# Performance work log

Measured on AMD Instinct MI355X. Metric: run time of the kernel, lower is better.

Reference implementation:

```python
import jax, jax.numpy as jnp
import numpy as np

HIDDEN = 1024
NUM_HEADS = 16
HEAD_DIM = 64
B, S = 2, 2048


def setup_inputs() -> dict:
    key = jax.random.key(0)
    k1, k2, k3 = jax.random.split(key, 3)
    x = jax.random.normal(k1, (B, S, HIDDEN), dtype=jnp.float32)
    # xavier-uniform style scaling for the projection weights
    lim_qkv = (6.0 / (HIDDEN + 3 * NUM_HEADS * HEAD_DIM)) ** 0.5
    lim_o = (6.0 / (NUM_HEADS * HEAD_DIM + HIDDEN)) ** 0.5
    w_qkv = jax.random.uniform(k2, (HIDDEN, 3 * NUM_HEADS * HEAD_DIM), jnp.float32, -lim_qkv, lim_qkv)
    w_o = jax.random.uniform(k3, (NUM_HEADS * HEAD_DIM, HIDDEN), jnp.float32, -lim_o, lim_o)
    return {"x": x, "w_qkv": w_qkv, "w_o": w_o}


def reference(x, w_qkv, w_o):
    b, s, _ = x.shape
    qkv = jnp.einsum('bsh,hf->bsf', x, w_qkv)               # [b, s, 3*H*D]
    qkv = qkv.reshape(b, s, 3, NUM_HEADS, HEAD_DIM)
    q = jnp.transpose(qkv[:, :, 0], (0, 2, 1, 3))           # [b, h, s, d]
    k = jnp.transpose(qkv[:, :, 1], (0, 2, 3, 1))           # [b, h, d, s]
    v = jnp.transpose(qkv[:, :, 2], (0, 2, 1, 3))           # [b, h, s, d]
    scores = jnp.einsum('bhqd,bhdk->bhqk', q, k) / jnp.sqrt(jnp.float32(HEAD_DIM))
    scores = jax.nn.softmax(scores, axis=-1)                # [b, h, q, k]
    # NOTE: faithful to source bug: sums over q, output indexed by k
    values = jnp.einsum('bhqk,bhkd->bhkd', scores, v)       # [b, h, s, d]
    values = jnp.transpose(values, (0, 2, 1, 3)).reshape(b, s, NUM_HEADS * HEAD_DIM)
    return jnp.einsum('bsf,fh->bsh', values, w_o)
```

## Files before the change

kernel.cpp:

```cpp
#include <hip/hip_runtime.h>
#include <stdint.h>


#define DEV static __device__ __forceinline__

typedef unsigned short u16;
typedef __attribute__((ext_vector_type(4))) float f32x4;
typedef __attribute__((ext_vector_type(16))) float f32x16;
typedef __bf16 bf16x8 __attribute__((ext_vector_type(8)));
typedef __attribute__((ext_vector_type(8))) unsigned short u16x8;
typedef __attribute__((ext_vector_type(4))) unsigned short u16x4;

#define QSCALE 0.18033688011112042f

DEV u16 f2bf(float f) {
    unsigned u = __builtin_bit_cast(unsigned, f);
    u += 0x7fffu + ((u >> 16) & 1u);
    return (u16)(u >> 16);
}
DEV float bf2f(u16 h) {
    unsigned u = ((unsigned)h) << 16;
    return __builtin_bit_cast(float, u);
}

DEV void async_copy16(const void* g, void* l) {
    __builtin_amdgcn_global_load_lds(
        (__attribute__((address_space(1))) void*)(g),
        (__attribute__((address_space(3))) void*)(l), 16, 0, 0);
}

DEV void transpose_tile(const float* __restrict__ src, u16* __restrict__ dst,
                        int rows, int cols, int bx, int by, int t, float* tile) {
    int c0 = bx * 32, r0 = by * 32;
    int tx = t & 31, ty = t >> 5;
#pragma unroll
    for (int i = 0; i < 4; i++)
        tile[(ty + i * 8) * 33 + tx] = src[(size_t)(r0 + ty + i * 8) * cols + c0 + tx];
    __syncthreads();
#pragma unroll
    for (int i = 0; i < 4; i++)
        dst[(size_t)(c0 + ty + i * 8) * rows + r0 + tx] = f2bf(tile[tx * 33 + ty + i * 8]);
}

__global__ __launch_bounds__(256) void prep(
    const float* __restrict__ x, const float* __restrict__ wqkv,
    const float* __restrict__ wo, u16* __restrict__ xb,
    u16* __restrict__ wqkvT, u16* __restrict__ woT) {
    __shared__ float tile[32 * 33];
    const int gid = blockIdx.x;
    const int t = threadIdx.x;
    if (gid < 4096) {
        int i = gid * 256 + t;
        f32x4 v = *(const f32x4*)(x + (size_t)i * 4);
        u16x4 o;
#pragma unroll
        for (int j = 0; j < 4; j++) o[j] = f2bf(v[j]);
        *(u16x4*)(xb + (size_t)i * 4) = o;
    } else if (gid < 7168) {
        int lid = gid - 4096;
        transpose_tile(wqkv, wqkvT, 1024, 3072, lid % 96, lid / 96, t, tile);
    } else {
        int lid = gid - 7168;
        transpose_tile(wo, woT, 1024, 1024, lid & 31, lid >> 5, t, tile);
    }
}

__global__ __launch_bounds__(256) void gemm_qkv(
    const u16* __restrict__ A, const u16* __restrict__ Bt,
    u16* __restrict__ qb, u16* __restrict__ kb, u16* __restrict__ vb) {
    __shared__ __align__(16) u16 smem[128 * 136];
    u16* As = smem;
    u16* Bs = smem + 4096;
    const int t = threadIdx.x;
    const int wave = t >> 6;
    const int lane = t & 63;
    const int quad = lane >> 4;
    const int l16 = lane & 15;
    const int wr = wave >> 1;
    const int wc = wave & 1;
    const int m0 = blockIdx.y * 128;
    const int n0 = blockIdx.x * 128;

    f32x4 acc[4][4];
#pragma unroll
    for (int i = 0; i < 4; i++)
#pragma unroll
        for (int j = 0; j < 4; j++) acc[i][j] = {0.f, 0.f, 0.f, 0.f};

    for (int kt = 0; kt < 1024; kt += 32) {
#pragma unroll
        for (int i = 0; i < 2; i++) {
            int idx = i * 256 + t;
            int row = idx >> 2, kc = idx & 3;
            async_copy16(A + (size_t)(m0 + row) * 1024 + kt + kc * 8, &As[idx * 8]);
            async_copy16(Bt + (size_t)(n0 + row) * 1024 + kt + kc * 8, &Bs[idx * 8]);
        }
        __syncthreads();
        bf16x8 af[4], bfr[4];
#pragma unroll
        for (int mt = 0; mt < 4; mt++)
            af[mt] = *(const bf16x8*)&As[(wr * 64 + mt * 16 + l16) * 32 + quad * 8];
#pragma unroll
        for (int nt = 0; nt < 4; nt++)
            bfr[nt] = *(const bf16x8*)&Bs[(wc * 64 + nt * 16 + l16) * 32 + quad * 8];
#pragma unroll
        for (int mt = 0; mt < 4; mt++)
#pragma unroll
            for (int nt = 0; nt < 4; nt++)
                acc[mt][nt] = __builtin_amdgcn_mfma_f32_16x16x32_bf16(
                    af[mt], bfr[nt], acc[mt][nt], 0, 0, 0);
        __syncthreads();
    }

    const int tsel = n0 >> 10;
    u16* dst = tsel == 0 ? qb : (tsel == 1 ? kb : vb);
    const float scl = tsel == 0 ? QSCALE : 1.0f;
#pragma unroll
    for (int mt = 0; mt < 4; mt++)
#pragma unroll
        for (int nt = 0; nt < 4; nt++) {
            int nn = wc * 64 + nt * 16 + l16;
#pragma unroll
            for (int r = 0; r < 4; r++) {
                int mm = wr * 64 + mt * 16 + quad * 4 + r;
                smem[mm * 136 + nn] = f2bf(acc[mt][nt][r] * scl);
            }
        }
    __syncthreads();
    const int col0 = (l16) * 8;
    const int rowb = (t >> 4);
    const int h0 = (n0 & 1023) >> 6;
#pragma unroll
    for (int i = 0; i < 8; i++) {
        int row = i * 16 + rowb;
        u16x8 v = *(const u16x8*)&smem[row * 136 + col0];
        int h = h0 + (col0 >> 6), d = col0 & 63;
        int mm = m0 + row;
        int b = mm >> 11, s = mm & 2047;
        *(u16x8*)&dst[((size_t)((b * 16 + h) * 2048 + s)) * 64 + d] = v;
    }
}

__global__ __launch_bounds__(256) void attn_pass1(
    const u16* __restrict__ qb, const u16* __restrict__ kb,
    float* __restrict__ lp) {
    __shared__ __align__(16) u16 Ks0[256 * 32];
    __shared__ __align__(16) u16 Ks1[256 * 32];
    const int t = threadIdx.x;
    const int wave = t >> 6;
    const int lane = t & 63;
    const int l32 = lane & 31, half = lane >> 5;
    const int kchunk = blockIdx.x & 1;
    const int qblk = (blockIdx.x >> 1) & 15;
    const int bh = blockIdx.x >> 5;
    const int q0 = qblk * 128 + wave * 32;

    const u16* Qr = qb + (size_t)(bh * 2048 + q0 + l32) * 64 + half * 8;
    bf16x8 a[4];
#pragma unroll
    for (int f = 0; f < 4; f++) a[f] = *(const bf16x8*)&Qr[f * 16];

    const u16* Kbase = kb + (size_t)(bh * 2048 + kchunk * 1024) * 64;
    const int srow = t >> 2, sc = (t & 3) * 8;

    float lsum[16];
#pragma unroll
    for (int r = 0; r < 16; r++) lsum[r] = 0.f;

    for (int kt = 0; kt < 4; kt++) {
#pragma unroll
        for (int rr = 0; rr < 4; rr++) {
            const u16* src = Kbase + (size_t)(kt * 256 + rr * 64 + srow) * 64 + sc;
            async_copy16(src, &Ks0[rr * 2048 + t * 8]);
            async_copy16(src + 32, &Ks1[rr * 2048 + t * 8]);
        }
        __syncthreads();
#pragma unroll
        for (int sub = 0; sub < 8; sub++) {
            const int row = sub * 32 + l32;
            bf16x8 bfr[4];
            bfr[0] = *(const bf16x8*)&Ks0[row * 32 + half * 8];
            bfr[1] = *(const bf16x8*)&Ks0[row * 32 + 16 + half * 8];
            bfr[2] = *(const bf16x8*)&Ks1[row * 32 + half * 8];
            bfr[3] = *(const bf16x8*)&Ks1[row * 32 + 16 + half * 8];
            f32x16 acc;
#pragma unroll
            for (int r = 0; r < 16; r++) acc[r] = 0.f;
#pragma unroll
            for (int f = 0; f < 4; f++)
                acc = __builtin_amdgcn_mfma_f32_32x32x16_bf16(a[f], bfr[f], acc, 0, 0, 0);
#pragma unroll
            for (int r = 0; r < 16; r++)
                lsum[r] += __builtin_amdgcn_exp2f(acc[r]);
        }
        __syncthreads();
    }
#pragma unroll
    for (int r = 0; r < 16; r++) {
        float v = lsum[r];
        v += __shfl_xor(v, 1);
        v += __shfl_xor(v, 2);
        v += __shfl_xor(v, 4);
        v += __shfl_xor(v, 8);
        v += __shfl_xor(v, 16);
        lsum[r] = v;
    }
    if (l32 == 0) {
        float* dst = lp + kchunk * 65536 + bh * 2048 + q0 + half * 4;
#pragma unroll
        for (int r = 0; r < 16; r++)
            dst[(r & 3) + 8 * (r >> 2)] = lsum[r];
    }
}

__global__ __launch_bounds__(256) void attn_pass2(
    const u16* __restrict__ qb, const u16* __restrict__ kb,
    const float* __restrict__ lp, float* __restrict__ cp) {
    __shared__ __align__(16) u16 Qs0[256 * 32];
    __shared__ __align__(16) u16 Qs1[256 * 32];
    __shared__ __align__(16) float li_lds[1024];
    const int t = threadIdx.x;
    const int wave = t >> 6;
    const int lane = t & 63;
    const int l32 = lane & 31, half = lane >> 5;
    const int qchunk = blockIdx.x & 1;
    const int kblk = (blockIdx.x >> 1) & 15;
    const int bh = blockIdx.x >> 5;
    const int k0 = kblk * 128 + wave * 32;

    {
        const int base = bh * 2048 + qchunk * 1024;
        f32x4 p0 = *(const f32x4*)&lp[base + t * 4];
        f32x4 p1 = *(const f32x4*)&lp[65536 + base + t * 4];
        f32x4 li;
#pragma unroll
        for (int j = 0; j < 4; j++) li[j] = 1.0f / (p0[j] + p1[j]);
        *(f32x4*)&li_lds[t * 4] = li;
    }

    const u16* Kr = kb + (size_t)(bh * 2048 + k0 + l32) * 64 + half * 8;
    bf16x8 b[4];
#pragma unroll
    for (int f = 0; f < 4; f++) b[f] = *(const bf16x8*)&Kr[f * 16];

    const u16* Qbase = qb + (size_t)(bh * 2048 + qchunk * 1024) * 64;
    const int srow = t >> 2, sc = (t & 3) * 8;

    float cs = 0.f;
    __syncthreads();

    for (int qt = 0; qt < 4; qt++) {
#pragma unroll
        for (int rr = 0; rr < 4; rr++) {
            const u16* src = Qbase + (size_t)(qt * 256 + rr * 64 + srow) * 64 + sc;
            async_copy16(src, &Qs0[rr * 2048 + t * 8]);
            async_copy16(src + 32, &Qs1[rr * 2048 + t * 8]);
        }
        __syncthreads();
#pragma unroll
        for (int sub = 0; sub < 8; sub++) {
            const int row = sub * 32 + l32;
            bf16x8 af[4];
            af[0] = *(const bf16x8*)&Qs0[row * 32 + half * 8];
            af[1] = *(const bf16x8*)&Qs0[row * 32 + 16 + half * 8];
            af[2] = *(const bf16x8*)&Qs1[row * 32 + half * 8];
            af[3] = *(const bf16x8*)&Qs1[row * 32 + 16 + half * 8];
            f32x16 acc;
#pragma unroll
            for (int r = 0; r < 16; r++) acc[r] = 0.f;
#pragma unroll
            for (int f = 0; f < 4; f++)
                acc = __builtin_amdgcn_mfma_f32_32x32x16_bf16(af[f], b[f], acc, 0, 0, 0);
            const float* lr = &li_lds[qt * 256 + sub * 32 + half * 4];
            f32x4 li0 = *(const f32x4*)&lr[0];
            f32x4 li1 = *(const f32x4*)&lr[8];
            f32x4 li2 = *(const f32x4*)&lr[16];
            f32x4 li3 = *(const f32x4*)&lr[24];
#pragma unroll
            for (int r = 0; r < 4; r++) cs += __builtin_amdgcn_exp2f(acc[r]) * li0[r];
#pragma unroll
            for (int r = 0; r < 4; r++) cs += __builtin_amdgcn_exp2f(acc[4 + r]) * li1[r];
#pragma unroll
            for (int r = 0; r < 4; r++) cs += __builtin_amdgcn_exp2f(acc[8 + r]) * li2[r];
#pragma unroll
            for (int r = 0; r < 4; r++) cs += __builtin_amdgcn_exp2f(acc[12 + r]) * li3[r];
        }
        __syncthreads();
    }
    cs += __shfl_xor(cs, 32);
    if (lane < 32)
        cp[qchunk * 65536 + bh * 2048 + k0 + lane] = cs;
}

__global__ __launch_bounds__(256) void gemm_out(
    const u16* __restrict__ vb, const float* __restrict__ cp,
    const u16* __restrict__ Bt, float* __restrict__ out) {
    __shared__ __align__(16) u16 As[64 * 32];
    __shared__ __align__(16) u16 Bs[128 * 32];
    const int m0 = blockIdx.y * 64;
    const int n0 = blockIdx.x * 128;
    const int t = threadIdx.x;
    const int wave = t >> 6, lane = t & 63;
    const int quad = lane >> 4, l16 = lane & 15;
    const int wr = wave >> 1, wc = wave & 1;

    const int mm = m0 + (t >> 2);
    const int b = mm >> 11, s = mm & 2047;

    f32x4 acc[2][4];
#pragma unroll
    for (int i = 0; i < 2; i++)
#pragma unroll
        for (int j = 0; j < 4; j++) acc[i][j] = {0.f, 0.f, 0.f, 0.f};

    for (int kt = 0; kt < 1024; kt += 32) {
        {
            int k0 = kt + (t & 3) * 8;
            int h = k0 >> 6, d = k0 & 63;
            int ci = (b * 16 + h) * 2048 + s;
            float csc = cp[ci] + cp[65536 + ci];
            u16x8 v = *(const u16x8*)&vb[((size_t)ci) * 64 + d];
            u16x8 o;
#pragma unroll
            for (int j = 0; j < 8; j++) o[j] = f2bf(bf2f(v[j]) * csc);
            *(u16x8*)&As[t * 8] = o;
        }
#pragma unroll
        for (int i = 0; i < 2; i++) {
            int idx = i * 256 + t;
            int row = idx >> 2, kc = idx & 3;
            async_copy16(Bt + (size_t)(n0 + row) * 1024 + kt + kc * 8, &Bs[idx * 8]);
        }
        __syncthreads();
        bf16x8 af[2], bfr[4];
#pragma unroll
        for (int mt = 0; mt < 2; mt++)
            af[mt] = *(const bf16x8*)&As[(wr * 32 + mt * 16 + l16) * 32 + quad * 8];
#pragma unroll
        for (int nt = 0; nt < 4; nt++)
            bfr[nt] = *(const bf16x8*)&Bs[(wc * 64 + nt * 16 + l16) * 32 + quad * 8];
#pragma unroll
        for (int mt = 0; mt < 2; mt++)
#pragma unroll
            for (int nt = 0; nt < 4; nt++)
                acc[mt][nt] = __builtin_amdgcn_mfma_f32_16x16x32_bf16(
                    af[mt], bfr[nt], acc[mt][nt], 0, 0, 0);
        __syncthreads();
    }
#pragma unroll
    for (int nt = 0; nt < 4; nt++) {
        int nn = n0 + wc * 64 + nt * 16 + l16;
#pragma unroll
        for (int mt = 0; mt < 2; mt++) {
#pragma unroll
            for (int r = 0; r < 4; r++) {
                int mr = m0 + wr * 32 + mt * 16 + quad * 4 + r;
                out[(size_t)mr * 1024 + nn] = acc[mt][nt][r];
            }
        }
    }
}


extern "C" void kernel_launch(void* const* d_in, const int* in_sizes, int n_in,
                              void* d_out, int out_size, void* d_ws, size_t ws_size,
                              hipStream_t stream) {
    const float* x    = (const float*)d_in[0];
    const float* wqkv = (const float*)d_in[1];
    const float* wo   = (const float*)d_in[2];
    float* out = (float*)d_out;
    char* ws = (char*)d_ws;

    u16* xb      = (u16*)(ws);
    u16* wqkvT   = (u16*)(ws + 8388608);
    u16* woT     = (u16*)(ws + 14680064);
    u16* qb      = (u16*)(ws + 16777216);
    u16* kb      = (u16*)(ws + 25165824);
    u16* vb      = (u16*)(ws + 33554432);
    float* lp    = (float*)(ws);
    float* cp    = (float*)(ws + 1048576);

    prep<<<8192, 256, 0, stream>>>(x, wqkv, wo, xb, wqkvT, woT);
    gemm_qkv<<<dim3(24, 32), 256, 0, stream>>>(xb, wqkvT, qb, kb, vb);
    attn_pass1<<<1024, 256, 0, stream>>>(qb, kb, lp);
    attn_pass2<<<1024, 256, 0, stream>>>(qb, kb, lp, cp);
    gemm_out<<<dim3(8, 64), 256, 0, stream>>>(vb, cp, woT, out);
}
```

Baseline: 200.2 us.

## XOR-swizzle LDS tiles and software-pipeline exp2 in attention passes

Applies an XOR swizzle to the 16-byte chunk index when filling LDS tiles in the QKV GEMM, both attention passes and the output GEMM, and applies the matching swizzle on the MFMA operand reads. The aim is to remove LDS bank conflicts caused by the 64-byte row stride. In the attention passes, the exp2 reduction of each sub-tile is also delayed by one iteration, so the transcendental work overlaps with the next MFMA chain. This costs extra registers for the double-buffered accumulators.

```diff
diff --git a/kernel.cpp b/kernel.cpp
--- a/kernel.cpp
+++ b/kernel.cpp
@@ -28,6 +28,7 @@
         (__attribute__((address_space(1))) void*)(g),
         (__attribute__((address_space(3))) void*)(l), 16, 0, 0);
 }
+
 
 DEV void transpose_tile(const float* __restrict__ src, u16* __restrict__ dst,
                         int rows, int cols, int bx, int by, int t, float* tile) {
@@ -80,6 +81,7 @@
     const int wc = wave & 1;
     const int m0 = blockIdx.y * 128;
     const int n0 = blockIdx.x * 128;
+    const int swz = (l16 >> 1) & 3;
 
     f32x4 acc[4][4];
 #pragma unroll
@@ -91,7 +93,7 @@
 #pragma unroll
         for (int i = 0; i < 2; i++) {
             int idx = i * 256 + t;
-            int row = idx >> 2, kc = idx & 3;
+            int row = idx >> 2, kc = (idx & 3) ^ ((idx >> 3) & 3);
             async_copy16(A + (size_t)(m0 + row) * 1024 + kt + kc * 8, &As[idx * 8]);
             async_copy16(Bt + (size_t)(n0 + row) * 1024 + kt + kc * 8, &Bs[idx * 8]);
         }
@@ -99,10 +101,10 @@
         bf16x8 af[4], bfr[4];
 #pragma unroll
         for (int mt = 0; mt < 4; mt++)
-            af[mt] = *(const bf16x8*)&As[(wr * 64 + mt * 16 + l16) * 32 + quad * 8];
+            af[mt] = *(const bf16x8*)&As[(wr * 64 + mt * 16 + l16) * 32 + (quad ^ swz) * 8];
 #pragma unroll
         for (int nt = 0; nt < 4; nt++)
-            bfr[nt] = *(const bf16x8*)&Bs[(wc * 64 + nt * 16 + l16) * 32 + quad * 8];
+            bfr[nt] = *(const bf16x8*)&Bs[(wc * 64 + nt * 16 + l16) * 32 + (quad ^ swz) * 8];
 #pragma unroll
         for (int mt = 0; mt < 4; mt++)
 #pragma unroll
@@ -154,6 +156,9 @@
     const int qblk = (blockIdx.x >> 1) & 15;
     const int bh = blockIdx.x >> 5;
     const int q0 = qblk * 128 + wave * 32;
+    const int swz = (l32 >> 1) & 3;
+    const int c0 = ((half ^ swz) & 3) * 8;
+    const int c1 = (((2 + half) ^ swz) & 3) * 8;
 
     const u16* Qr = qb + (size_t)(bh * 2048 + q0 + l32) * 64 + half * 8;
     bf16x8 a[4];
@@ -161,7 +166,7 @@
     for (int f = 0; f < 4; f++) a[f] = *(const bf16x8*)&Qr[f * 16];
 
     const u16* Kbase = kb + (size_t)(bh * 2048 + kchunk * 1024) * 64;
-    const int srow = t >> 2, sc = (t & 3) * 8;
+    const int srow = t >> 2, sc = ((t & 3) ^ ((t >> 3) & 3)) * 8;
 
     float lsum[16];
 #pragma unroll
@@ -175,23 +180,34 @@
             async_copy16(src + 32, &Ks1[rr * 2048 + t * 8]);
         }
         __syncthreads();
+        f32x16 acc2[2];
 #pragma unroll
         for (int sub = 0; sub < 8; sub++) {
             const int row = sub * 32 + l32;
             bf16x8 bfr[4];
-            bfr[0] = *(const bf16x8*)&Ks0[row * 32 + half * 8];
-            bfr[1] = *(const bf16x8*)&Ks0[row * 32 + 16 + half * 8];
-            bfr[2] = *(const bf16x8*)&Ks1[row * 32 + half * 8];
-            bfr[3] = *(const bf16x8*)&Ks1[row * 32 + 16 + half * 8];
+            bfr[0] = *(const bf16x8*)&Ks0[row * 32 + c0];
+            bfr[1] = *(const bf16x8*)&Ks0[row * 32 + c1];
+            bfr[2] = *(const bf16x8*)&Ks1[row * 32 + c0];
+            bfr[3] = *(const bf16x8*)&Ks1[row * 32 + c1];
             f32x16 acc;
 #pragma unroll
             for (int r = 0; r < 16; r++) acc[r] = 0.f;
 #pragma unroll
             for (int f = 0; f < 4; f++)
                 acc = __builtin_amdgcn_mfma_f32_32x32x16_bf16(a[f], bfr[f], acc, 0, 0, 0);
+            acc2[sub & 1] = acc;
+            if (sub > 0) {
+                f32x16 p = acc2[(sub - 1) & 1];
+#pragma unroll
+                for (int r = 0; r < 16; r++)
+                    lsum[r] += __builtin_amdgcn_exp2f(p[r]);
+            }
+        }
+        {
+            f32x16 p = acc2[1];
 #pragma unroll
             for (int r = 0; r < 16; r++)
-                lsum[r] += __builtin_amdgcn_exp2f(acc[r]);
+                lsum[r] += __builtin_amdgcn_exp2f(p[r]);
         }
         __syncthreads();
     }
@@ -227,6 +243,9 @@
     const int kblk = (blockIdx.x >> 1) & 15;
     const int bh = blockIdx.x >> 5;
     const int k0 = kblk * 128 + wave * 32;
+    const int swz = (l32 >> 1) & 3;
+    const int c0 = ((half ^ swz) & 3) * 8;
+    const int c1 = (((2 + half) ^ swz) & 3) * 8;
 
     {
         const int base = bh * 2048 + qchunk * 1024;
@@ -244,7 +263,7 @@
     for (int f = 0; f < 4; f++) b[f] = *(const bf16x8*)&Kr[f * 16];
 
     const u16* Qbase = qb + (size_t)(bh * 2048 + qchunk * 1024) * 64;
-    const int srow = t >> 2, sc = (t & 3) * 8;
+    const int srow = t >> 2, sc = ((t & 3) ^ ((t >> 3) & 3)) * 8;
 
     float cs = 0.f;
     __syncthreads();
@@ -257,33 +276,44 @@
             async_copy16(src + 32, &Qs1[rr * 2048 + t * 8]);
         }
         __syncthreads();
+        f32x16 acc2[2];
 #pragma unroll
         for (int sub = 0; sub < 8; sub++) {
             const int row = sub * 32 + l32;
             bf16x8 af[4];
-            af[0] = *(const bf16x8*)&Qs0[row * 32 + half * 8];
-            af[1] = *(const bf16x8*)&Qs0[row * 32 + 16 + half * 8];
-            af[2] = *(const bf16x8*)&Qs1[row * 32 + half * 8];
-            af[3] = *(const bf16x8*)&Qs1[row * 32 + 16 + half * 8];
+            af[0] = *(const bf16x8*)&Qs0[row * 32 + c0];
+            af[1] = *(const bf16x8*)&Qs0[row * 32 + c1];
+            af[2] = *(const bf16x8*)&Qs1[row * 32 + c0];
+            af[3] = *(const bf16x8*)&Qs1[row * 32 + c1];
             f32x16 acc;
 #pragma unroll
             for (int r = 0; r < 16; r++) acc[r] = 0.f;
 #pragma unroll
             for (int f = 0; f < 4; f++)
                 acc = __builtin_amdgcn_mfma_f32_32x32x16_bf16(af[f], b[f], acc, 0, 0, 0);
-            const float* lr = &li_lds[qt * 256 + sub * 32 + half * 4];
-            f32x4 li0 = *(const f32x4*)&lr[0];
-            f32x4 li1 = *(const f32x4*)&lr[8];
-            f32x4 li2 = *(const f32x4*)&lr[16];
-            f32x4 li3 = *(const f32x4*)&lr[24];
-#pragma unroll
-            for (int r = 0; r < 4; r++) cs += __builtin_amdgcn_exp2f(acc[r]) * li0[r];
-#pragma unroll
-            for (int r = 0; r < 4; r++) cs += __builtin_amdgcn_exp2f(acc[4 + r]) * li1[r];
-#pragma unroll
-            for (int r = 0; r < 4; r++) cs += __builtin_amdgcn_exp2f(acc[8 + r]) * li2[r];
-#pragma unroll
-            for (int r = 0; r < 4; r++) cs += __builtin_amdgcn_exp2f(acc[12 + r]) * li3[r];
+            acc2[sub & 1] = acc;
+            if (sub > 0) {
+                f32x16 p = acc2[(sub - 1) & 1];
+                const float* lr = &li_lds[qt * 256 + (sub - 1) * 32 + half * 4];
+#pragma unroll
+                for (int g = 0; g < 4; g++) {
+                    f32x4 li = *(const f32x4*)&lr[g * 8];
+#pragma unroll
+                    for (int r = 0; r < 4; r++)
+                        cs += __builtin_amdgcn_exp2f(p[g * 4 + r]) * li[r];
+                }
+            }
+        }
+        {
+            f32x16 p = acc2[1];
+            const float* lr = &li_lds[qt * 256 + 7 * 32 + half * 4];
+#pragma unroll
+            for (int g = 0; g < 4; g++) {
+                f32x4 li = *(const f32x4*)&lr[g * 8];
+#pragma unroll
+                for (int r = 0; r < 4; r++)
+                    cs += __builtin_amdgcn_exp2f(p[g * 4 + r]) * li[r];
+            }
         }
         __syncthreads();
     }
@@ -303,9 +333,11 @@
     const int wave = t >> 6, lane = t & 63;
     const int quad = lane >> 4, l16 = lane & 15;
     const int wr = wave >> 1, wc = wave & 1;
+    const int swz = (l16 >> 1) & 3;
 
     const int mm = m0 + (t >> 2);
     const int b = mm >> 11, s = mm & 2047;
+    const int cswz = (t & 3) ^ ((t >> 3) & 3);
 
     f32x4 acc[2][4];
 #pragma unroll
@@ -315,7 +347,7 @@
 
     for (int kt = 0; kt < 1024; kt += 32) {
         {
-            int k0 = kt + (t & 3) * 8;
+            int k0 = kt + cswz * 8;
             int h = k0 >> 6, d = k0 & 63;
             int ci = (b * 16 + h) * 2048 + s;
             float csc = cp[ci] + cp[65536 + ci];
@@ -328,17 +360,17 @@
 #pragma unroll
         for (int i = 0; i < 2; i++) {
             int idx = i * 256 + t;
-            int row = idx >> 2, kc = idx & 3;
+            int row = idx >> 2, kc = (idx & 3) ^ ((idx >> 3) & 3);
             async_copy16(Bt + (size_t)(n0 + row) * 1024 + kt + kc * 8, &Bs[idx * 8]);
         }
         __syncthreads();
         bf16x8 af[2], bfr[4];
 #pragma unroll
         for (int mt = 0; mt < 2; mt++)
-            af[mt] = *(const bf16x8*)&As[(wr * 32 + mt * 16 + l16) * 32 + quad * 8];
+            af[mt] = *(const bf16x8*)&As[(wr * 32 + mt * 16 + l16) * 32 + (quad ^ swz) * 8];
 #pragma unroll
         for (int nt = 0; nt < 4; nt++)
-            bfr[nt] = *(const bf16x8*)&Bs[(wc * 64 + nt * 16 + l16) * 32 + quad * 8];
+            bfr[nt] = *(const bf16x8*)&Bs[(wc * 64 + nt * 16 + l16) * 32 + (quad ^ swz) * 8];
 #pragma unroll
         for (int mt = 0; mt < 2; mt++)
 #pragma unroll
```

New measurement: 209.1 us. 1.04x slower.
